# Optimization experiments

Measured on AMD Instinct MI355X. Metric: run time of the kernel, lower is better.

Reference implementation:

```python
import jax, jax.numpy as jnp
import numpy as np

L, H, P = 16384, 1024, 512
DT_MIN, DT_MAX = 1e-3, 1e-1
STEP_RESCALE = 1.0


def setup_inputs() -> dict:
    key = jax.random.key(0)
    ks = jax.random.split(key, 7)
    input_sequence = jax.random.normal(ks[0], (L, H), jnp.float32)
    # eigenvalues with negative real part (left half plane), HiPPO-like imag parts
    Lambda_re = -(jax.random.uniform(ks[1], (P,), jnp.float32) * 0.9 + 0.1)
    Lambda_im = jnp.pi * jnp.arange(P, dtype=jnp.float32)
    B = jax.random.normal(ks[2], (P, H, 2), jnp.float32) / jnp.sqrt(2.0 * H)   # real/imag of B_tilde (P,H)
    C = jax.random.normal(ks[3], (H, P, 2), jnp.float32) / jnp.sqrt(2.0 * P)   # real/imag of C_tilde (H,P)
    D = jax.random.normal(ks[4], (H,), jnp.float32)
    u01 = jax.random.uniform(ks[5], (P, 1), jnp.float32)
    log_step = jnp.log(DT_MIN) + u01 * (jnp.log(DT_MAX) - jnp.log(DT_MIN))     # (P,1)
    return dict(input_sequence=input_sequence, Lambda_re=Lambda_re, Lambda_im=Lambda_im,
                B=B, C=C, D=D, log_step=log_step)


def _binop(q_i, q_j):
    # diagonal linear recurrence composition: (A, b) pairs
    A_i, b_i = q_i
    A_j, b_j = q_j
    return A_j * A_i, A_j * b_i + b_j


def reference(input_sequence, Lambda_re, Lambda_im, B, C, D, log_step):
    Lambda = Lambda_re + 1j * Lambda_im                        # (P,) complex64
    B_tilde = B[..., 0] + 1j * B[..., 1]                       # (P,H)
    C_tilde = C[..., 0] + 1j * C[..., 1]                       # (H,P)
    step = STEP_RESCALE * jnp.exp(log_step[:, 0])              # (P,)
    # ZOH discretization
    Lambda_bar = jnp.exp(Lambda * step)                        # (P,)
    B_bar = ((Lambda_bar - 1.0) / Lambda)[:, None] * B_tilde   # (P,H)
    # Bu_elements: (L,P) complex
    Bu = input_sequence.astype(B_bar.dtype) @ B_bar.T
    Lambda_elems = jnp.broadcast_to(Lambda_bar, Bu.shape)      # (L,P)
    # parallel associative scan over the diagonal recurrence x_t = Lambda_bar*x_{t-1} + Bu_t
    _, xs = jax.lax.associative_scan(_binop, (Lambda_elems, Bu))
    ys = 2.0 * (xs @ C_tilde.T).real                           # conj_sym => factor 2, (L,H)
    return ys + D * input_sequence
```

## Files before the change

kernel.cpp:

```cpp
#include <hip/hip_runtime.h>
#include <math.h>

#define L_SEQ 16384
#define H_DIM 1024
#define P_DIM 512
#define N2P   1024
#define KDIM  1024
#define NKT   16
#define CHUNK 64
#define NCHUNK 256

typedef __attribute__((ext_vector_type(8))) short short8;
typedef __attribute__((ext_vector_type(4))) float f32x4;
typedef __attribute__((address_space(3))) const char* lds3_t;

__device__ __forceinline__ unsigned short f2bf(float f){
    unsigned int u = __float_as_uint(f);
    u = (u + 0x7FFFu + ((u >> 16) & 1u)) >> 16;
    return (unsigned short)u;
}
__device__ __forceinline__ float bf2f(unsigned int lo16){
    return __uint_as_float(lo16 << 16);
}

__global__ void k_prep_lambda(const float* __restrict__ lre, const float* __restrict__ lim,
                              const float* __restrict__ lstep,
                              float* __restrict__ lam, float* __restrict__ coef,
                              float* __restrict__ lpow)
{
    int p = threadIdx.x;
    double step = exp((double)lstep[p]);
    double dr = (double)lre[p], di = (double)lim[p];
    double ar = dr*step, ai = di*step;
    double er = exp(ar);
    double lbr = er*cos(ai), lbi = er*sin(ai);
    lam[2*p] = (float)lbr; lam[2*p+1] = (float)lbi;
    double nr = lbr - 1.0, ni = lbi;
    double d2 = dr*dr + di*di;
    coef[2*p]   = (float)((nr*dr + ni*di)/d2);
    coef[2*p+1] = (float)((ni*dr - nr*di)/d2);
    double xr = lbr, xi = lbi;
    #pragma unroll
    for (int s=0;s<6;s++){ double t = xr*xr - xi*xi; xi = 2.0*xr*xi; xr = t; }
    lpow[2*p] = (float)xr; lpow[2*p+1] = (float)xi;
}

__global__ __launch_bounds__(256)
void k_prep_BB(const float* __restrict__ B, const float* __restrict__ coef,
               unsigned short* __restrict__ BB)
{
    int i = blockIdx.x*256 + threadIdx.x;
    int p = i >> 10, h = i & 1023;
    float br = B[2*i], bi = B[2*i+1];
    float cr = coef[2*p], ci = coef[2*p+1];
    BB[(size_t)(2*p)*H_DIM + h]   = f2bf(cr*br - ci*bi);
    BB[(size_t)(2*p+1)*H_DIM + h] = f2bf(cr*bi + ci*br);
}

__global__ __launch_bounds__(256)
void k_prep_CC(const float* __restrict__ C, unsigned short* __restrict__ CC)
{
    int i = blockIdx.x*256 + threadIdx.x;
    int h = i >> 9, p = i & 511;
    float cr = C[2*i], ci = C[2*i+1];
    CC[(size_t)h*N2P + 2*p]     = f2bf(2.f*cr);
    CC[(size_t)h*N2P + 2*p + 1] = f2bf(-2.f*ci);
}

__global__ __launch_bounds__(256)
void k_cast(const float4* __restrict__ u, unsigned short* __restrict__ o)
{
    int i = blockIdx.x*256 + threadIdx.x;
    float4 a = u[2*i], b = u[2*i+1];
    union { short8 v; unsigned short s[8]; } r;
    r.s[0]=f2bf(a.x); r.s[1]=f2bf(a.y); r.s[2]=f2bf(a.z); r.s[3]=f2bf(a.w);
    r.s[4]=f2bf(b.x); r.s[5]=f2bf(b.y); r.s[6]=f2bf(b.z); r.s[7]=f2bf(b.w);
    *reinterpret_cast<short8*>(o + (size_t)i*8) = r.v;
}

template<int EPI>
__global__ __launch_bounds__(512, 2)
void gemm256(const unsigned short* __restrict__ A, const unsigned short* __restrict__ Bm,
             float* __restrict__ Cf, unsigned short* __restrict__ Cb,
             const float* __restrict__ Dv, const unsigned short* __restrict__ U16)
{
    __shared__ char lds[131072];
    const int tid  = threadIdx.x;
    const int lane = tid & 63;
    const int wid  = tid >> 6;
    const int wm = wid >> 2, wn = wid & 3;
    const int wg = ((int)blockIdx.x & 7) * 32 + ((int)blockIdx.x >> 3);
    const int tm = wg >> 2, tn = wg & 3;
    const int lr = lane & 15;

    const int scol = ((tid & 7) ^ ((tid >> 3) & 7)) << 3;
    const int srow = tid >> 3;
    const int kc0 = (((lane >> 4)      ^ (lr & 7)) << 4);
    const int kc1 = ((((lane >> 4) | 4) ^ (lr & 7)) << 4);
    const int aSub = wm*16384 + lr*128;
    const int bSub = 32768 + (wn >> 1)*16384 + (wn & 1)*8192 + lr*128;

#define GLOAD(SRC, DST) __builtin_amdgcn_global_load_lds( \
        (const __attribute__((address_space(1))) void*)(SRC), \
        (__attribute__((address_space(3))) void*)(DST), 16, 0, 0)
#define STAGE_A(kt_, h_) do{ \
    char* d_ = lds + (((kt_)&1)<<16) + (h_)*16384 + tid*16; \
    const unsigned short* s_ = A + (size_t)(tm*256 + (h_)*128 + srow)*KDIM + (size_t)(kt_)*64 + scol; \
    GLOAD(s_, d_); GLOAD(s_ + (size_t)64*KDIM, d_ + 8192); }while(0)
#define STAGE_B(kt_, h_) do{ \
    char* d_ = lds + (((kt_)&1)<<16) + 32768 + (h_)*16384 + tid*16; \
    const unsigned short* s_ = Bm + (size_t)(tn*256 + (h_)*128 + srow)*KDIM + (size_t)(kt_)*64 + scol; \
    GLOAD(s_, d_); GLOAD(s_ + (size_t)64*KDIM, d_ + 8192); }while(0)
#define DSR(D, P, IMM) asm volatile("ds_read_b128 %0, %1 offset:" IMM : "=v"(D) : "v"(P))
#define LGKM0 do{ asm volatile("s_waitcnt lgkmcnt(0)" ::: "memory"); \
                  __builtin_amdgcn_sched_barrier(0); }while(0)
#define VMC4  asm volatile("s_waitcnt vmcnt(4)" ::: "memory")
#define MFMA(a,b,c) __builtin_amdgcn_mfma_f32_16x16x32_bf16(a,b,c,0,0,0)
#define BAR __builtin_amdgcn_s_barrier()
#define PRIO1 __builtin_amdgcn_s_setprio(1)
#define PRIO0 __builtin_amdgcn_s_setprio(0)

    short8 a1[4], a2[4], bb0[4], bb1[4];
    f32x4 acc[8][4];
    #pragma unroll
    for (int m=0;m<8;m++)
        #pragma unroll
        for (int n=0;n<4;n++) acc[m][n] = (f32x4){0.f,0.f,0.f,0.f};

    STAGE_A(0,0); STAGE_A(0,1); STAGE_B(0,0); STAGE_B(0,1); STAGE_B(1,0); STAGE_B(1,1);
    VMC4; BAR;

    for (int kt = 0; kt < NKT; ++kt) {
        const int sb = (kt & 1) << 16;
        const int tA = (kt+1 < NKT) ? kt+1 : NKT-1;
        const int tB = (kt+2 < NKT) ? kt+2 : NKT-1;
        lds3_t pa0 = (lds3_t)(lds + sb + aSub + kc0);
        lds3_t pa1 = (lds3_t)(lds + sb + aSub + kc1);
        lds3_t pb0 = (lds3_t)(lds + sb + bSub + kc0);
        lds3_t pb1 = (lds3_t)(lds + sb + bSub + kc1);

        DSR(a1[0], pa0, "0");    DSR(a1[1], pa0, "2048");
        DSR(a1[2], pa0, "4096"); DSR(a1[3], pa0, "6144");
        DSR(bb0[0], pb0, "0");    DSR(bb0[1], pb0, "2048");
        DSR(bb0[2], pb0, "4096"); DSR(bb0[3], pb0, "6144");
        STAGE_A(tA, 0);
        BAR; LGKM0; PRIO1;
        #pragma unroll
        for (int m=0;m<4;m++)
            #pragma unroll
            for (int n=0;n<4;n++) acc[m][n] = MFMA(a1[m], bb0[n], acc[m][n]);
        PRIO0; BAR;

        DSR(a2[0], pa0, "8192");  DSR(a2[1], pa0, "10240");
        DSR(a2[2], pa0, "12288"); DSR(a2[3], pa0, "14336");
        STAGE_A(tA, 1);
        BAR; LGKM0; PRIO1;
        #pragma unroll
        for (int m=0;m<4;m++)
            #pragma unroll
            for (int n=0;n<4;n++) acc[4+m][n] = MFMA(a2[m], bb0[n], acc[4+m][n]);
        PRIO0; BAR;

        DSR(a1[0], pa1, "0");    DSR(a1[1], pa1, "2048");
        DSR(a1[2], pa1, "4096"); DSR(a1[3], pa1, "6144");
        DSR(bb1[0], pb1, "0");    DSR(bb1[1], pb1, "2048");
        DSR(bb1[2], pb1, "4096"); DSR(bb1[3], pb1, "6144");
        BAR; LGKM0; PRIO1;
        #pragma unroll
        for (int m=0;m<4;m++)
            #pragma unroll
            for (int n=0;n<4;n++) acc[m][n] = MFMA(a1[m], bb1[n], acc[m][n]);
        PRIO0; BAR;

        DSR(a2[0], pa1, "8192");  DSR(a2[1], pa1, "10240");
        DSR(a2[2], pa1, "12288"); DSR(a2[3], pa1, "14336");
        STAGE_B(tB, 0); STAGE_B(tB, 1);
        VMC4;
        BAR; LGKM0; PRIO1;
        #pragma unroll
        for (int m=0;m<4;m++)
            #pragma unroll
            for (int n=0;n<4;n++) acc[4+m][n] = MFMA(a2[m], bb1[n], acc[4+m][n]);
        PRIO0; BAR;
    }
    asm volatile("s_waitcnt vmcnt(0)" ::: "memory");

    const int orow0 = tm*256 + wm*128 + (lane>>4)*4;
    const int ocol0 = tn*256 + wn*64 + lr;
    #pragma unroll
    for (int m=0;m<8;m++){
        #pragma unroll
        for (int n=0;n<4;n++){
            int row = orow0 + m*16, col = ocol0 + n*16;
            #pragma unroll
            for (int j=0;j<4;j++){
                size_t idx = (size_t)(row + j)*N2P + col;
                if (EPI) Cf[idx] = acc[m][n][j] + Dv[col]*bf2f(U16[idx]);
                else     Cb[idx] = f2bf(acc[m][n][j]);
            }
        }
    }
#undef GLOAD
#undef STAGE_A
#undef STAGE_B
#undef DSR
#undef LGKM0
#undef VMC4
#undef MFMA
#undef BAR
#undef PRIO1
#undef PRIO0
}

__global__ __launch_bounds__(512)
void k_agg(const unsigned int* __restrict__ Bu, const float* __restrict__ lam,
           float* __restrict__ agg)
{
    int p = threadIdx.x, c = blockIdx.x;
    float lrr = lam[2*p], lii = lam[2*p+1];
    float xr = 0.f, xi = 0.f;
    const unsigned int* b2 = Bu + (size_t)c*CHUNK*512 + p;
    #pragma unroll 4
    for (int t=0;t<CHUNK;t++){
        unsigned int b = b2[(size_t)t*512];
        float br = __uint_as_float(b << 16);
        float bi = __uint_as_float(b & 0xffff0000u);
        float tr = lrr*xr - lii*xi + br;
        xi = lrr*xi + lii*xr + bi;
        xr = tr;
    }
    agg[((size_t)c*P_DIM + p)*2]     = xr;
    agg[((size_t)c*P_DIM + p)*2 + 1] = xi;
}

__global__ __launch_bounds__(256)
void k_scan(const float* __restrict__ agg, const float* __restrict__ lpow,
            float* __restrict__ xinit)
{
    __shared__ float sr[NCHUNK], si[NCHUNK];
    int c = threadIdx.x, p = blockIdx.x;
    float xr = agg[((size_t)c*P_DIM + p)*2];
    float xi = agg[((size_t)c*P_DIM + p)*2 + 1];
    sr[c] = xr; si[c] = xi;
    float wr = lpow[2*p], wi = lpow[2*p+1];
    for (int s=1; s<NCHUNK; s<<=1){
        __syncthreads();
        float ur = 0.f, ui = 0.f;
        if (c >= s){ ur = sr[c-s]; ui = si[c-s]; }
        __syncthreads();
        xr += wr*ur - wi*ui;
        xi += wr*ui + wi*ur;
        sr[c] = xr; si[c] = xi;
        float t = wr*wr - wi*wi; wi = 2.f*wr*wi; wr = t;
    }
    __syncthreads();
    float er = 0.f, ei = 0.f;
    if (c > 0){ er = sr[c-1]; ei = si[c-1]; }
    xinit[((size_t)c*P_DIM + p)*2]     = er;
    xinit[((size_t)c*P_DIM + p)*2 + 1] = ei;
}

__global__ __launch_bounds__(512)
void k_apply(const unsigned int* __restrict__ Bu, const float* __restrict__ lam,
             const float* __restrict__ xinit, unsigned int* __restrict__ xs)
{
    int p = threadIdx.x, c = blockIdx.x;
    float lrr = lam[2*p], lii = lam[2*p+1];
    float xr = xinit[((size_t)c*P_DIM + p)*2];
    float xi = xinit[((size_t)c*P_DIM + p)*2 + 1];
    const unsigned int* b2 = Bu + (size_t)c*CHUNK*512 + p;
    unsigned int* o = xs + (size_t)c*CHUNK*512 + p;
    #pragma unroll 4
    for (int t=0;t<CHUNK;t++){
        unsigned int b = b2[(size_t)t*512];
        float br = __uint_as_float(b << 16);
        float bi = __uint_as_float(b & 0xffff0000u);
        float tr = lrr*xr - lii*xi + br;
        xi = lrr*xi + lii*xr + bi;
        xr = tr;
        o[(size_t)t*512] = (unsigned int)f2bf(xr) | ((unsigned int)f2bf(xi) << 16);
    }
}

extern "C" void kernel_launch(void* const* d_in, const int* in_sizes, int n_in,
                              void* d_out, int out_size, void* d_ws, size_t ws_size,
                              hipStream_t stream)
{
    const float* u   = (const float*)d_in[0];
    const float* lre = (const float*)d_in[1];
    const float* lim = (const float*)d_in[2];
    const float* B   = (const float*)d_in[3];
    const float* C   = (const float*)d_in[4];
    const float* D   = (const float*)d_in[5];
    const float* ls  = (const float*)d_in[6];
    float* out = (float*)d_out;

    char* w = (char*)d_ws;
    unsigned short* u16  = (unsigned short*)(w + 0);
    unsigned short* xs16 = (unsigned short*)(w + 33554432);
    unsigned short* Bu16 = (unsigned short*)(w + 67108864);
    unsigned short* BB   = (unsigned short*)(w + 100663296);
    unsigned short* CC   = (unsigned short*)(w + 102760448);
    float* lam   = (float*)(w + 104857600);
    float* coef  = (float*)(w + 104861696);
    float* lpow  = (float*)(w + 104865792);
    float* agg   = (float*)(w + 104869888);
    float* xinit = (float*)(w + 105918464);

    k_prep_lambda<<<1, P_DIM, 0, stream>>>(lre, lim, ls, lam, coef, lpow);
    k_prep_BB<<<(P_DIM*H_DIM)/256, 256, 0, stream>>>(B, coef, BB);
    k_prep_CC<<<(H_DIM*P_DIM)/256, 256, 0, stream>>>(C, CC);
    k_cast<<<(L_SEQ*H_DIM)/(256*8), 256, 0, stream>>>((const float4*)u, u16);

    gemm256<0><<<256, 512, 0, stream>>>(u16, BB, nullptr, Bu16, nullptr, nullptr);

    k_agg<<<NCHUNK, P_DIM, 0, stream>>>((const unsigned int*)Bu16, lam, agg);
    k_scan<<<P_DIM, NCHUNK, 0, stream>>>(agg, lpow, xinit);
    k_apply<<<NCHUNK, P_DIM, 0, stream>>>((const unsigned int*)Bu16, lam, xinit,
                                          (unsigned int*)xs16);

    gemm256<1><<<256, 512, 0, stream>>>(xs16, CC, out, nullptr, D, u16);
}
```

Measured before the change: 134.6 us.

## Cut barriers in GEMM main loop and overlap LDS reads with MFMA

The bf16 MFMA GEMM inner loop is rescheduled so each k-step uses two workgroup barriers instead of eight. Partial lgkmcnt waits let the next fragment's LDS reads stay in flight while the current MFMA block runs. Both A-tile prefetches are issued up front and the B-tile prefetch moves behind a single barrier, and the loop is unrolled by two. The aim is less barrier stall and better hiding of LDS latency, at the cost of fragile hand-placed wait counts and possibly more register pressure from the unroll.

```diff
diff --git a/kernel.cpp b/kernel.cpp
--- a/kernel.cpp
+++ b/kernel.cpp
@@ -112,11 +112,12 @@
     const unsigned short* s_ = Bm + (size_t)(tn*256 + (h_)*128 + srow)*KDIM + (size_t)(kt_)*64 + scol; \
     GLOAD(s_, d_); GLOAD(s_ + (size_t)64*KDIM, d_ + 8192); }while(0)
 #define DSR(D, P, IMM) asm volatile("ds_read_b128 %0, %1 offset:" IMM : "=v"(D) : "v"(P))
-#define LGKM0 do{ asm volatile("s_waitcnt lgkmcnt(0)" ::: "memory"); \
-                  __builtin_amdgcn_sched_barrier(0); }while(0)
+#define LGKM(N) do{ asm volatile("s_waitcnt lgkmcnt(" #N ")" ::: "memory"); \
+                    __builtin_amdgcn_sched_barrier(0); }while(0)
 #define VMC4  asm volatile("s_waitcnt vmcnt(4)" ::: "memory")
+#define ABAR  asm volatile("s_barrier" ::: "memory")
+#define SB0   __builtin_amdgcn_sched_barrier(0)
 #define MFMA(a,b,c) __builtin_amdgcn_mfma_f32_16x16x32_bf16(a,b,c,0,0,0)
-#define BAR __builtin_amdgcn_s_barrier()
 #define PRIO1 __builtin_amdgcn_s_setprio(1)
 #define PRIO0 __builtin_amdgcn_s_setprio(0)
 
@@ -128,8 +129,9 @@
         for (int n=0;n<4;n++) acc[m][n] = (f32x4){0.f,0.f,0.f,0.f};
 
     STAGE_A(0,0); STAGE_A(0,1); STAGE_B(0,0); STAGE_B(0,1); STAGE_B(1,0); STAGE_B(1,1);
-    VMC4; BAR;
-
+    VMC4; ABAR;
+
+    #pragma unroll 2
     for (int kt = 0; kt < NKT; ++kt) {
         const int sb = (kt & 1) << 16;
         const int tA = (kt+1 < NKT) ? kt+1 : NKT-1;
@@ -143,45 +145,47 @@
         DSR(a1[2], pa0, "4096"); DSR(a1[3], pa0, "6144");
         DSR(bb0[0], pb0, "0");    DSR(bb0[1], pb0, "2048");
         DSR(bb0[2], pb0, "4096"); DSR(bb0[3], pb0, "6144");
-        STAGE_A(tA, 0);
-        BAR; LGKM0; PRIO1;
-        #pragma unroll
-        for (int m=0;m<4;m++)
-            #pragma unroll
-            for (int n=0;n<4;n++) acc[m][n] = MFMA(a1[m], bb0[n], acc[m][n]);
-        PRIO0; BAR;
-
+        STAGE_A(tA, 0); STAGE_A(tA, 1);
         DSR(a2[0], pa0, "8192");  DSR(a2[1], pa0, "10240");
         DSR(a2[2], pa0, "12288"); DSR(a2[3], pa0, "14336");
-        STAGE_A(tA, 1);
-        BAR; LGKM0; PRIO1;
+        LGKM(4);
+        PRIO1;
         #pragma unroll
         for (int m=0;m<4;m++)
             #pragma unroll
-            for (int n=0;n<4;n++) acc[4+m][n] = MFMA(a2[m], bb0[n], acc[4+m][n]);
-        PRIO0; BAR;
-
+            for (int n=0;n<4;n++) acc[m][n] = MFMA(a1[m], bb0[n], acc[m][n]);
+        PRIO0; SB0;
         DSR(a1[0], pa1, "0");    DSR(a1[1], pa1, "2048");
         DSR(a1[2], pa1, "4096"); DSR(a1[3], pa1, "6144");
         DSR(bb1[0], pb1, "0");    DSR(bb1[1], pb1, "2048");
         DSR(bb1[2], pb1, "4096"); DSR(bb1[3], pb1, "6144");
-        BAR; LGKM0; PRIO1;
+        LGKM(8);
+        PRIO1;
         #pragma unroll
         for (int m=0;m<4;m++)
             #pragma unroll
-            for (int n=0;n<4;n++) acc[m][n] = MFMA(a1[m], bb1[n], acc[m][n]);
-        PRIO0; BAR;
-
+            for (int n=0;n<4;n++) acc[4+m][n] = MFMA(a2[m], bb0[n], acc[4+m][n]);
+        PRIO0; SB0;
         DSR(a2[0], pa1, "8192");  DSR(a2[1], pa1, "10240");
         DSR(a2[2], pa1, "12288"); DSR(a2[3], pa1, "14336");
+        LGKM(4);
+        ABAR;
         STAGE_B(tB, 0); STAGE_B(tB, 1);
+        PRIO1;
+        #pragma unroll
+        for (int m=0;m<4;m++)
+            #pragma unroll
+            for (int n=0;n<4;n++) acc[m][n] = MFMA(a1[m], bb1[n], acc[m][n]);
+        PRIO0; SB0;
+        LGKM(0);
+        PRIO1;
+        #pragma unroll
+        for (int m=0;m<4;m++)
+            #pragma unroll
+            for (int n=0;n<4;n++) acc[4+m][n] = MFMA(a2[m], bb1[n], acc[4+m][n]);
+        PRIO0; SB0;
         VMC4;
-        BAR; LGKM0; PRIO1;
-        #pragma unroll
-        for (int m=0;m<4;m++)
-            #pragma unroll
-            for (int n=0;n<4;n++) acc[4+m][n] = MFMA(a2[m], bb1[n], acc[4+m][n]);
-        PRIO0; BAR;
+        ABAR;
     }
     asm volatile("s_waitcnt vmcnt(0)" ::: "memory");
 
@@ -204,10 +208,11 @@
 #undef STAGE_A
 #undef STAGE_B
 #undef DSR
-#undef LGKM0
+#undef LGKM
 #undef VMC4
+#undef ABAR
+#undef SB0
 #undef MFMA
-#undef BAR
 #undef PRIO1
 #undef PRIO0
 }
```

Measured after the change: 129.0 us. -4.2%, faster.
